# Kernel optimization log

Measured on AMD Instinct MI355X. Metric: run time of the kernel, lower is better.

The kernel has to match this reference:

```python
import jax, jax.numpy as jnp
import numpy as np

E = 16        # n_experts
K = 2         # n_active_experts
D = 2048      # d_model
F = 1408      # ffn_hidden
B, S = 4, 2048


def _swiglu(x, wg, wu, wd):
    # x: [N, D]; wg/wu: [F, D]; wd: [D, F]
    return (jax.nn.silu(x @ wg.T) * (x @ wu.T)) @ wd.T


def setup_inputs() -> dict:
    key = jax.random.key(0)
    ks = jax.random.split(key, 8)
    sc = 0.02
    return {
        "x": jax.random.normal(ks[0], (B, S, D), jnp.float32),
        "gate_w": jax.random.normal(ks[1], (E, D), jnp.float32) * sc,
        "w_gate": jax.random.normal(ks[2], (E, F, D), jnp.float32) * sc,
        "w_up": jax.random.normal(ks[3], (E, F, D), jnp.float32) * sc,
        "w_down": jax.random.normal(ks[4], (E, D, F), jnp.float32) * sc,
        "sw_gate": jax.random.normal(ks[5], (F, D), jnp.float32) * sc,
        "sw_up": jax.random.normal(ks[6], (F, D), jnp.float32) * sc,
        "sw_down": jax.random.normal(ks[7], (D, F), jnp.float32) * sc,
        "expert_bias": jnp.zeros((E,), jnp.float32),
    }


def reference(x, gate_w, w_gate, w_up, w_down, sw_gate, sw_up, sw_down, expert_bias):
    b, s, d = x.shape
    flat = x.reshape(-1, d)                           # [N, D]
    logits = flat @ gate_w.T                          # [N, E]
    probs = jax.nn.softmax(logits, axis=-1)
    biased = logits + expert_bias
    _, top_idx = jax.lax.top_k(biased, K)             # [N, K] int32
    top_w = jnp.take_along_axis(probs, top_idx, axis=-1)
    top_w = top_w / jnp.sum(top_w, axis=-1, keepdims=True)
    # scatter top-k weights into a dense per-expert combine matrix [N, E]
    combine = jnp.sum(jax.nn.one_hot(top_idx, E, dtype=flat.dtype) * top_w[..., None], axis=1)
    out = jnp.zeros_like(flat)
    for e in range(E):  # fixed small expert loop
        out = out + combine[:, e:e + 1] * _swiglu(flat, w_gate[e], w_up[e], w_down[e])
    out = out + _swiglu(flat, sw_gate, sw_up, sw_down)  # shared expert
    return out.reshape(b, s, d)
```

## Files before the change

kernel.cpp:

```cpp
#include <hip/hip_runtime.h>
#include <hip/hip_bf16.h>
#include <cstdint>

#define NE 16
#define D_ 2048
#define F_ 1408
#define NTOK 8192
#define NPAIR (NTOK * 2)
#define SHARED_BASE NPAIR
#define NTOT (NPAIR + NTOK)

#define BM1 256
#define BN1 128
#define BK 64
#define NF1 (F_ / BN1)
#define NF2 (D_ / BN1)
#define MAXRT 111

typedef __attribute__((ext_vector_type(8))) short short8;
typedef __attribute__((ext_vector_type(4))) float f32x4;

static __device__ __forceinline__ ushort f2bf(float f) {
    union { float f; unsigned u; } v; v.f = f;
    unsigned u = v.u;
    return (ushort)((u + 0x7FFFu + ((u >> 16) & 1u)) >> 16);
}

static __device__ __forceinline__ float bf2f(ushort u) {
    union { unsigned u; float f; } v; v.u = ((unsigned)u) << 16;
    return v.f;
}

static __device__ __forceinline__ void cvt_store8(ushort* dst, const float* src) {
    const float4* s = reinterpret_cast<const float4*>(src);
    float4 a = s[0], b = s[1];
    short8 v;
    v[0] = (short)f2bf(a.x); v[1] = (short)f2bf(a.y);
    v[2] = (short)f2bf(a.z); v[3] = (short)f2bf(a.w);
    v[4] = (short)f2bf(b.x); v[5] = (short)f2bf(b.y);
    v[6] = (short)f2bf(b.z); v[7] = (short)f2bf(b.w);
    *reinterpret_cast<short8*>(dst) = v;
}

static __device__ __forceinline__ void gll16(const void* g, void* l) {
    __builtin_amdgcn_global_load_lds((const __attribute__((address_space(1))) void*)g,
                                     (__attribute__((address_space(3))) void*)l, 16, 0, 0);
}

__global__ __launch_bounds__(256) void k_cvt(const float* __restrict__ src,
                                             ushort* __restrict__ dst, int n8) {
    int i = blockIdx.x * 256 + threadIdx.x;
    int stride = gridDim.x * 256;
    for (; i < n8; i += stride) cvt_store8(dst + (size_t)i * 8, src + (size_t)i * 8);
}

__global__ __launch_bounds__(256) void k_route(const float* __restrict__ x,
                                               const float* __restrict__ gate_w,
                                               const float* __restrict__ expert_bias,
                                               int* __restrict__ topk_idx,
                                               float* __restrict__ topk_w) {
    const int wave = threadIdx.x >> 6;
    const int lane = threadIdx.x & 63;
    const int tok = blockIdx.x * 4 + wave;
    if (tok >= NTOK) return;
    const float* xr = x + (size_t)tok * D_;
    float xv[D_ / 64];
#pragma unroll
    for (int i = 0; i < D_ / 64; ++i) xv[i] = xr[lane + 64 * i];

    float logits[NE];
#pragma unroll
    for (int e = 0; e < NE; ++e) {
        const float* gw = gate_w + e * D_;
        float p = 0.f;
#pragma unroll
        for (int i = 0; i < D_ / 64; ++i) p += xv[i] * gw[lane + 64 * i];
#pragma unroll
        for (int off = 32; off > 0; off >>= 1) p += __shfl_xor(p, off, 64);
        logits[e] = p;
    }
    int i1 = 0; float b1 = logits[0] + expert_bias[0];
#pragma unroll
    for (int e = 1; e < NE; ++e) {
        float b = logits[e] + expert_bias[e];
        if (b > b1) { b1 = b; i1 = e; }
    }
    int i2 = -1; float b2 = -3.4e38f;
#pragma unroll
    for (int e = 0; e < NE; ++e) {
        if (e == i1) continue;
        float b = logits[e] + expert_bias[e];
        if (b > b2) { b2 = b; i2 = e; }
    }
    float l1 = logits[i1], l2 = logits[i2];
    float m = fmaxf(l1, l2);
    float e1 = __expf(l1 - m), e2 = __expf(l2 - m);
    float s = e1 + e2;
    if (lane == 0) {
        topk_idx[tok * 2 + 0] = i1;
        topk_idx[tok * 2 + 1] = i2;
        topk_w[tok * 2 + 0] = e1 / s;
        topk_w[tok * 2 + 1] = e2 / s;
    }
}

__global__ void k_zero_meta(int* meta) {
    if (threadIdx.x < 128) meta[threadIdx.x] = 0;
}

__global__ __launch_bounds__(256) void k_count(const int* __restrict__ topk_idx,
                                               int* __restrict__ meta) {
    int t = blockIdx.x * 256 + threadIdx.x;
    if (t >= NTOK) return;
    atomicAdd(&meta[topk_idx[t * 2 + 0]], 1);
    atomicAdd(&meta[topk_idx[t * 2 + 1]], 1);
}

__global__ void k_prefix(int* meta) {
    if (threadIdx.x == 0) {
        int acc = 0;
        for (int e = 0; e < NE; ++e) { meta[32 + e] = acc; acc += meta[e]; }
        meta[32 + NE] = acc;
        int t = 0;
        for (int e = 0; e < NE; ++e) { meta[64 + e] = t; t += (meta[e] + BM1 - 1) / BM1; }
        meta[64 + NE] = t;
        meta[64 + NE + 1] = t + NTOK / BM1;
    }
}

__global__ __launch_bounds__(256) void k_scatter(const int* __restrict__ topk_idx,
                                                 const float* __restrict__ topk_w,
                                                 int* __restrict__ meta,
                                                 int* __restrict__ tok_sorted,
                                                 float* __restrict__ w_sorted,
                                                 int* __restrict__ inv) {
    int t = blockIdx.x * 256 + threadIdx.x;
    if (t >= NTOK) return;
#pragma unroll
    for (int k = 0; k < 2; ++k) {
        int e = topk_idx[t * 2 + k];
        int p = atomicAdd(&meta[16 + e], 1);
        int idx = meta[32 + e] + p;
        tok_sorted[idx] = t;
        w_sorted[idx] = topk_w[t * 2 + k];
        inv[t * 2 + k] = idx;
    }
}

static __device__ __forceinline__ bool grid_decode(const int* meta, int bid, int NF,
                                                   int& e, int& row0, int& fx) {
    if (bid >= meta[64 + NE + 1] * NF) return false;
    e = (bid >= meta[64 + NE] * NF) ? NE : 0;
    if (e == 0) {
#pragma unroll
        for (int i = 1; i < NE; ++i) if (bid >= meta[64 + i] * NF) e = i;
    }
    const int tile_base = meta[64 + e];
    const int nrt = meta[64 + e + 1] - tile_base;
    const int bw = bid - tile_base * NF;
    fx = bw / nrt;
    row0 = (bw - fx * nrt) * BM1;
    return true;
}

__global__ __launch_bounds__(512, 2) void k_ffn1(const ushort* __restrict__ xb,
                                                 const ushort* __restrict__ wgb,
                                                 const ushort* __restrict__ wub,
                                                 const ushort* __restrict__ swgb,
                                                 const ushort* __restrict__ swub,
                                                 const int* __restrict__ meta,
                                                 const int* __restrict__ tok_sorted,
                                                 const float* __restrict__ w_sorted,
                                                 ushort* __restrict__ Hbuf) {
    int e, row0, fx;
    if (!grid_decode(meta, blockIdx.x, NF1, e, row0, fx)) return;
    int n_e, base;
    if (e < NE) { n_e = meta[e]; base = meta[32 + e]; }
    else        { n_e = NTOK;    base = SHARED_BASE; }
    const int f0 = fx * BN1;
    const ushort* wg = (e < NE) ? wgb + (size_t)e * F_ * D_ : swgb;
    const ushort* wu = (e < NE) ? wub + (size_t)e * F_ * D_ : swub;

    __shared__ __align__(16) ushort As[2][BM1 * BK];
    __shared__ __align__(16) ushort Gs[2][BN1 * BK];
    __shared__ __align__(16) ushort Us[2][BN1 * BK];
    __shared__ int tks[BM1];
    __shared__ float tws[BM1];

    const int tid = threadIdx.x;
    const int wv = tid >> 6, lane = tid & 63;
    if (tid < BM1) {
        int r = row0 + tid;
        if (r < n_e) {
            tks[tid] = (e < NE) ? tok_sorted[base + r] : r;
            tws[tid] = (e < NE) ? w_sorted[base + r] : 1.0f;
        } else { tks[tid] = 0; tws[tid] = 0.f; }
    }
    __syncthreads();

    const ushort* srcA[4]; const ushort* srcG[2]; const ushort* srcU[2];
#pragma unroll
    for (int j = 0; j < 4; ++j) {
        int c = j * 512 + wv * 64 + lane;
        int r = c >> 3;
        int col = ((c & 7) ^ (r & 7)) * 8;
        srcA[j] = xb + (size_t)tks[r] * D_ + col;
    }
#pragma unroll
    for (int j = 0; j < 2; ++j) {
        int c = j * 512 + wv * 64 + lane;
        int r = c >> 3;
        int col = ((c & 7) ^ (r & 7)) * 8;
        srcG[j] = wg + (size_t)(f0 + r) * D_ + col;
        srcU[j] = wu + (size_t)(f0 + r) * D_ + col;
    }

    auto stage = [&](int buf, int k0) {
        char* bA = (char*)(&As[buf][0]) + wv * 1024;
        char* bG = (char*)(&Gs[buf][0]) + wv * 1024;
        char* bU = (char*)(&Us[buf][0]) + wv * 1024;
        gll16(srcA[0] + k0, bA);         gll16(srcA[1] + k0, bA + 8192);
        gll16(srcA[2] + k0, bA + 16384); gll16(srcA[3] + k0, bA + 24576);
        gll16(srcG[0] + k0, bG);         gll16(srcG[1] + k0, bG + 8192);
        gll16(srcU[0] + k0, bU);         gll16(srcU[1] + k0, bU + 8192);
    };

    f32x4 accg[4][4] = {}; f32x4 accu[4][4] = {};
    const int wm = (wv >> 1) * 64, wn = (wv & 1) * 64;
    const int fr = lane & 15, fq = lane >> 4;
    const int sw = fr & 7;
    const int rc0 = ((fq ^ sw) * 8);
    const int rc1 = (((4 + fq) ^ sw) * 8);

    auto compute = [&](int buf) {
        const ushort* pA = As[buf];
        const ushort* pG = Gs[buf];
        const ushort* pU = Us[buf];
#pragma unroll
        for (int kk = 0; kk < 2; ++kk) {
            const int rc = kk ? rc1 : rc0;
            short8 af[4], gf[4], uf[4];
#pragma unroll
            for (int mi = 0; mi < 4; ++mi)
                af[mi] = *reinterpret_cast<const short8*>(&pA[(wm + mi * 16 + fr) * BK + rc]);
#pragma unroll
            for (int ni = 0; ni < 4; ++ni) {
                gf[ni] = *reinterpret_cast<const short8*>(&pG[(wn + ni * 16 + fr) * BK + rc]);
                uf[ni] = *reinterpret_cast<const short8*>(&pU[(wn + ni * 16 + fr) * BK + rc]);
            }
#pragma unroll
            for (int mi = 0; mi < 4; ++mi)
#pragma unroll
                for (int ni = 0; ni < 4; ++ni) {
                    accg[mi][ni] = __builtin_amdgcn_mfma_f32_16x16x32_bf16(af[mi], gf[ni], accg[mi][ni], 0, 0, 0);
                    accu[mi][ni] = __builtin_amdgcn_mfma_f32_16x16x32_bf16(af[mi], uf[ni], accu[mi][ni], 0, 0, 0);
                }
        }
    };

    const int NK = D_ / BK;
    stage(0, 0);
    stage(1, BK);
    asm volatile("s_waitcnt vmcnt(8)" ::: "memory");
    __builtin_amdgcn_s_barrier();
    __builtin_amdgcn_sched_barrier(0);
    int cur = 0;
    for (int ks = 0; ks < NK; ++ks) {
        compute(cur);
        __builtin_amdgcn_s_barrier();
        if (ks + 2 < NK) {
            stage(cur, (ks + 2) * BK);
            asm volatile("s_waitcnt vmcnt(8)" ::: "memory");
        } else if (ks + 1 < NK) {
            asm volatile("s_waitcnt vmcnt(0)" ::: "memory");
        }
        __builtin_amdgcn_s_barrier();
        __builtin_amdgcn_sched_barrier(0);
        cur ^= 1;
    }

#pragma unroll
    for (int mi = 0; mi < 4; ++mi) {
#pragma unroll
        for (int r = 0; r < 4; ++r) {
            int lr = wm + mi * 16 + fq * 4 + r;
            int grow = row0 + lr;
            if (grow < n_e) {
                float w = tws[lr];
                ushort* hrow = Hbuf + (size_t)(base + grow) * F_ + f0 + wn;
#pragma unroll
                for (int ni = 0; ni < 4; ++ni) {
                    float g = accg[mi][ni][r];
                    float u = accu[mi][ni][r];
                    float h = w * (g / (1.f + __expf(-g))) * u;
                    hrow[ni * 16 + fr] = f2bf(h);
                }
            }
        }
    }
}

__global__ __launch_bounds__(512, 2) void k_ffn2(const ushort* __restrict__ Hbuf,
                                                 const ushort* __restrict__ wdb,
                                                 const ushort* __restrict__ swdb,
                                                 const int* __restrict__ meta,
                                                 ushort* __restrict__ Obuf) {
    int e, row0, dx;
    if (!grid_decode(meta, blockIdx.x, NF2, e, row0, dx)) return;
    int n_e, base;
    if (e < NE) { n_e = meta[e]; base = meta[32 + e]; }
    else        { n_e = NTOK;    base = SHARED_BASE; }
    const int d0 = dx * BN1;
    const ushort* wd = (e < NE) ? wdb + (size_t)e * D_ * F_ : swdb;

    __shared__ __align__(16) ushort As[2][BM1 * BK];
    __shared__ __align__(16) ushort Bs[2][BN1 * BK];

    const int tid = threadIdx.x;
    const int wv = tid >> 6, lane = tid & 63;

    const ushort* srcA[4]; const ushort* srcB[2];
#pragma unroll
    for (int j = 0; j < 4; ++j) {
        int c = j * 512 + wv * 64 + lane;
        int r = c >> 3;
        int col = ((c & 7) ^ (r & 7)) * 8;
        srcA[j] = Hbuf + (size_t)(base + row0 + r) * F_ + col;
    }
#pragma unroll
    for (int j = 0; j < 2; ++j) {
        int c = j * 512 + wv * 64 + lane;
        int r = c >> 3;
        int col = ((c & 7) ^ (r & 7)) * 8;
        srcB[j] = wd + (size_t)(d0 + r) * F_ + col;
    }

    auto stage = [&](int buf, int k0) {
        char* bA = (char*)(&As[buf][0]) + wv * 1024;
        char* bB = (char*)(&Bs[buf][0]) + wv * 1024;
        gll16(srcA[0] + k0, bA);         gll16(srcA[1] + k0, bA + 8192);
        gll16(srcA[2] + k0, bA + 16384); gll16(srcA[3] + k0, bA + 24576);
        gll16(srcB[0] + k0, bB);         gll16(srcB[1] + k0, bB + 8192);
    };

    f32x4 acc[4][4] = {};
    const int wm = (wv >> 1) * 64, wn = (wv & 1) * 64;
    const int fr = lane & 15, fq = lane >> 4;
    const int sw = fr & 7;
    const int rc0 = ((fq ^ sw) * 8);
    const int rc1 = (((4 + fq) ^ sw) * 8);

    auto compute = [&](int buf) {
        const ushort* pA = As[buf];
        const ushort* pB = Bs[buf];
#pragma unroll
        for (int kk = 0; kk < 2; ++kk) {
            const int rc = kk ? rc1 : rc0;
            short8 af[4], bfr[4];
#pragma unroll
            for (int mi = 0; mi < 4; ++mi)
                af[mi] = *reinterpret_cast<const short8*>(&pA[(wm + mi * 16 + fr) * BK + rc]);
#pragma unroll
            for (int ni = 0; ni < 4; ++ni)
                bfr[ni] = *reinterpret_cast<const short8*>(&pB[(wn + ni * 16 + fr) * BK + rc]);
#pragma unroll
            for (int mi = 0; mi < 4; ++mi)
#pragma unroll
                for (int ni = 0; ni < 4; ++ni)
                    acc[mi][ni] = __builtin_amdgcn_mfma_f32_16x16x32_bf16(af[mi], bfr[ni], acc[mi][ni], 0, 0, 0);
        }
    };

    const int NK = F_ / BK;
    stage(0, 0);
    stage(1, BK);
    asm volatile("s_waitcnt vmcnt(6)" ::: "memory");
    __builtin_amdgcn_s_barrier();
    __builtin_amdgcn_sched_barrier(0);
    int cur = 0;
    for (int ks = 0; ks < NK; ++ks) {
        compute(cur);
        __builtin_amdgcn_s_barrier();
        if (ks + 2 < NK) {
            stage(cur, (ks + 2) * BK);
            asm volatile("s_waitcnt vmcnt(6)" ::: "memory");
        } else if (ks + 1 < NK) {
            asm volatile("s_waitcnt vmcnt(0)" ::: "memory");
        }
        __builtin_amdgcn_s_barrier();
        __builtin_amdgcn_sched_barrier(0);
        cur ^= 1;
    }

#pragma unroll
    for (int mi = 0; mi < 4; ++mi) {
#pragma unroll
        for (int r = 0; r < 4; ++r) {
            int lr = wm + mi * 16 + fq * 4 + r;
            int slot = row0 + lr;
            if (slot < n_e) {
                ushort* orow = Obuf + (size_t)(base + slot) * D_ + d0 + wn;
#pragma unroll
                for (int ni = 0; ni < 4; ++ni)
                    orow[ni * 16 + fr] = f2bf(acc[mi][ni][r]);
            }
        }
    }
}

__global__ __launch_bounds__(256) void k_gather(const ushort* __restrict__ Obuf,
                                                const int* __restrict__ inv,
                                                float* __restrict__ out) {
    const int t = blockIdx.x;
    const int c = threadIdx.x * 8;
    const int s1 = inv[t * 2 + 0];
    const int s2 = inv[t * 2 + 1];
    short8 a = *reinterpret_cast<const short8*>(&Obuf[(size_t)s1 * D_ + c]);
    short8 b = *reinterpret_cast<const short8*>(&Obuf[(size_t)s2 * D_ + c]);
    short8 d = *reinterpret_cast<const short8*>(&Obuf[(size_t)(SHARED_BASE + t) * D_ + c]);
    float4 o0, o1;
    o0.x = bf2f((ushort)a[0]) + bf2f((ushort)b[0]) + bf2f((ushort)d[0]);
    o0.y = bf2f((ushort)a[1]) + bf2f((ushort)b[1]) + bf2f((ushort)d[1]);
    o0.z = bf2f((ushort)a[2]) + bf2f((ushort)b[2]) + bf2f((ushort)d[2]);
    o0.w = bf2f((ushort)a[3]) + bf2f((ushort)b[3]) + bf2f((ushort)d[3]);
    o1.x = bf2f((ushort)a[4]) + bf2f((ushort)b[4]) + bf2f((ushort)d[4]);
    o1.y = bf2f((ushort)a[5]) + bf2f((ushort)b[5]) + bf2f((ushort)d[5]);
    o1.z = bf2f((ushort)a[6]) + bf2f((ushort)b[6]) + bf2f((ushort)d[6]);
    o1.w = bf2f((ushort)a[7]) + bf2f((ushort)b[7]) + bf2f((ushort)d[7]);
    float4* op = reinterpret_cast<float4*>(out + (size_t)t * D_ + c);
    op[0] = o0; op[1] = o1;
}

extern "C" void kernel_launch(void* const* d_in, const int* in_sizes, int n_in,
                              void* d_out, int out_size, void* d_ws, size_t ws_size,
                              hipStream_t stream) {
    const float* x        = (const float*)d_in[0];
    const float* gate_w   = (const float*)d_in[1];
    const float* w_gate   = (const float*)d_in[2];
    const float* w_up     = (const float*)d_in[3];
    const float* w_down   = (const float*)d_in[4];
    const float* sw_gate  = (const float*)d_in[5];
    const float* sw_up    = (const float*)d_in[6];
    const float* sw_down  = (const float*)d_in[7];
    const float* expert_bias = (const float*)d_in[8];
    float* out = (float*)d_out;

    const size_t NW = (size_t)NE * F_ * D_;
    const size_t NSW = (size_t)F_ * D_;
    const size_t NX = (size_t)NTOK * D_;

    char* ws = (char*)d_ws;
    size_t off = 0;
    ushort* xb   = (ushort*)(ws + off); off += NX * 2;
    ushort* wgb  = (ushort*)(ws + off); off += NW * 2;
    ushort* wub  = (ushort*)(ws + off); off += NW * 2;
    ushort* wdb  = (ushort*)(ws + off); off += NW * 2;
    ushort* swgb = (ushort*)(ws + off); off += NSW * 2;
    ushort* swub = (ushort*)(ws + off); off += NSW * 2;
    ushort* swdb = (ushort*)(ws + off); off += NSW * 2;
    ushort* Hbuf = (ushort*)(ws + off); off += (size_t)NTOT * F_ * 2;
    int* tok_sorted = (int*)(ws + off); off += NPAIR * sizeof(int);
    float* w_sorted = (float*)(ws + off); off += NPAIR * sizeof(float);
    int* topk_idx = (int*)(ws + off); off += NTOK * 2 * sizeof(int);
    float* topk_w = (float*)(ws + off); off += NTOK * 2 * sizeof(float);
    int* inv = (int*)(ws + off); off += NTOK * 2 * sizeof(int);
    int* meta = (int*)(ws + off); off += 512;

    ushort* Obuf = wgb;

    k_route<<<NTOK / 4, 256, 0, stream>>>(x, gate_w, expert_bias, topk_idx, topk_w);
    k_zero_meta<<<1, 128, 0, stream>>>(meta);
    k_count<<<NTOK / 256, 256, 0, stream>>>(topk_idx, meta);
    k_prefix<<<1, 1, 0, stream>>>(meta);
    k_scatter<<<NTOK / 256, 256, 0, stream>>>(topk_idx, topk_w, meta, tok_sorted, w_sorted, inv);

    auto cvt = [&](const float* s, ushort* d, size_t n) {
        int n8 = (int)(n / 8);
        int blocks = (n8 + 255) / 256;
        if (blocks > 4096) blocks = 4096;
        k_cvt<<<blocks, 256, 0, stream>>>(s, d, n8);
    };
    cvt(x, xb, NX);
    cvt(w_gate, wgb, NW);
    cvt(w_up, wub, NW);
    cvt(w_down, wdb, NW);
    cvt(sw_gate, swgb, NSW);
    cvt(sw_up, swub, NSW);
    cvt(sw_down, swdb, NSW);

    k_ffn1<<<MAXRT * NF1, 512, 0, stream>>>(xb, wgb, wub, swgb, swub,
                                            meta, tok_sorted, w_sorted, Hbuf);

    k_ffn2<<<MAXRT * NF2, 512, 0, stream>>>(Hbuf, wdb, swdb, meta, Obuf);

    k_gather<<<NTOK, 256, 0, stream>>>(Obuf, inv, out);
}
```

Baseline: 945.1 us.

## Halve K-tile to 32 with new LDS swizzle and raise occupancy to 4 blocks

Cuts the K tile of both FFN GEMM kernels from 64 to 32. The LDS footprint per block halves, so launch bounds now ask for 4 blocks of 512 threads per CU instead of 2. The LDS layout and load addressing are rewritten with a new swizzle (lds_idx) that pairs rows, so each 16x16x32 MFMA fragment load stays free of bank conflicts. The trade-off is twice as many K iterations and barriers, and a tighter register budget that may spill the 128 float accumulators of the gate/up kernel.

```diff
diff --git a/kernel.cpp b/kernel.cpp
--- a/kernel.cpp
+++ b/kernel.cpp
@@ -12,7 +12,7 @@
 
 #define BM1 256
 #define BN1 128
-#define BK 64
+#define BK 32
 #define NF1 (F_ / BN1)
 #define NF2 (D_ / BN1)
 #define MAXRT 111
@@ -45,6 +45,10 @@
 static __device__ __forceinline__ void gll16(const void* g, void* l) {
     __builtin_amdgcn_global_load_lds((const __attribute__((address_space(1))) void*)g,
                                      (__attribute__((address_space(3))) void*)l, 16, 0, 0);
+}
+
+static __device__ __forceinline__ int lds_idx(int r, int fq) {
+    return ((r >> 1) * 8 + (r & 1) * 4 + (fq ^ ((r >> 1) & 3))) * 8;
 }
 
 __global__ __launch_bounds__(256) void k_cvt(const float* __restrict__ src,
@@ -163,7 +167,7 @@
     return true;
 }
 
-__global__ __launch_bounds__(512, 2) void k_ffn1(const ushort* __restrict__ xb,
+__global__ __launch_bounds__(512, 4) void k_ffn1(const ushort* __restrict__ xb,
                                                  const ushort* __restrict__ wgb,
                                                  const ushort* __restrict__ wub,
                                                  const ushort* __restrict__ swgb,
@@ -198,70 +202,67 @@
     }
     __syncthreads();
 
-    const ushort* srcA[4]; const ushort* srcG[2]; const ushort* srcU[2];
-#pragma unroll
-    for (int j = 0; j < 4; ++j) {
-        int c = j * 512 + wv * 64 + lane;
-        int r = c >> 3;
-        int col = ((c & 7) ^ (r & 7)) * 8;
-        srcA[j] = xb + (size_t)tks[r] * D_ + col;
-    }
+    const ushort* srcA[2]; const ushort* srcG; const ushort* srcU;
 #pragma unroll
     for (int j = 0; j < 2; ++j) {
         int c = j * 512 + wv * 64 + lane;
-        int r = c >> 3;
-        int col = ((c & 7) ^ (r & 7)) * 8;
-        srcG[j] = wg + (size_t)(f0 + r) * D_ + col;
-        srcU[j] = wu + (size_t)(f0 + r) * D_ + col;
+        int gr = (c >> 3) * 2 + ((c >> 2) & 1);
+        int gj = (c & 3) ^ ((c >> 3) & 3);
+        srcA[j] = xb + (size_t)tks[gr] * D_ + gj * 8;
+    }
+    {
+        int c = wv * 64 + lane;
+        int gr = (c >> 3) * 2 + ((c >> 2) & 1);
+        int gj = (c & 3) ^ ((c >> 3) & 3);
+        srcG = wg + (size_t)(f0 + gr) * D_ + gj * 8;
+        srcU = wu + (size_t)(f0 + gr) * D_ + gj * 8;
     }
 
     auto stage = [&](int buf, int k0) {
         char* bA = (char*)(&As[buf][0]) + wv * 1024;
         char* bG = (char*)(&Gs[buf][0]) + wv * 1024;
         char* bU = (char*)(&Us[buf][0]) + wv * 1024;
-        gll16(srcA[0] + k0, bA);         gll16(srcA[1] + k0, bA + 8192);
-        gll16(srcA[2] + k0, bA + 16384); gll16(srcA[3] + k0, bA + 24576);
-        gll16(srcG[0] + k0, bG);         gll16(srcG[1] + k0, bG + 8192);
-        gll16(srcU[0] + k0, bU);         gll16(srcU[1] + k0, bU + 8192);
+        gll16(srcA[0] + k0, bA); gll16(srcA[1] + k0, bA + 8192);
+        gll16(srcG + k0, bG);
+        gll16(srcU + k0, bU);
     };
 
     f32x4 accg[4][4] = {}; f32x4 accu[4][4] = {};
     const int wm = (wv >> 1) * 64, wn = (wv & 1) * 64;
     const int fr = lane & 15, fq = lane >> 4;
-    const int sw = fr & 7;
-    const int rc0 = ((fq ^ sw) * 8);
-    const int rc1 = (((4 + fq) ^ sw) * 8);
+
+    int offA[4], offN[4];
+#pragma unroll
+    for (int mi = 0; mi < 4; ++mi) offA[mi] = lds_idx(wm + mi * 16 + fr, fq);
+#pragma unroll
+    for (int ni = 0; ni < 4; ++ni) offN[ni] = lds_idx(wn + ni * 16 + fr, fq);
 
     auto compute = [&](int buf) {
         const ushort* pA = As[buf];
         const ushort* pG = Gs[buf];
         const ushort* pU = Us[buf];
-#pragma unroll
-        for (int kk = 0; kk < 2; ++kk) {
-            const int rc = kk ? rc1 : rc0;
-            short8 af[4], gf[4], uf[4];
-#pragma unroll
-            for (int mi = 0; mi < 4; ++mi)
-                af[mi] = *reinterpret_cast<const short8*>(&pA[(wm + mi * 16 + fr) * BK + rc]);
+        short8 af[4], gf[4], uf[4];
+#pragma unroll
+        for (int mi = 0; mi < 4; ++mi)
+            af[mi] = *reinterpret_cast<const short8*>(&pA[offA[mi]]);
+#pragma unroll
+        for (int ni = 0; ni < 4; ++ni) {
+            gf[ni] = *reinterpret_cast<const short8*>(&pG[offN[ni]]);
+            uf[ni] = *reinterpret_cast<const short8*>(&pU[offN[ni]]);
+        }
+#pragma unroll
+        for (int mi = 0; mi < 4; ++mi)
 #pragma unroll
             for (int ni = 0; ni < 4; ++ni) {
-                gf[ni] = *reinterpret_cast<const short8*>(&pG[(wn + ni * 16 + fr) * BK + rc]);
-                uf[ni] = *reinterpret_cast<const short8*>(&pU[(wn + ni * 16 + fr) * BK + rc]);
+                accg[mi][ni] = __builtin_amdgcn_mfma_f32_16x16x32_bf16(af[mi], gf[ni], accg[mi][ni], 0, 0, 0);
+                accu[mi][ni] = __builtin_amdgcn_mfma_f32_16x16x32_bf16(af[mi], uf[ni], accu[mi][ni], 0, 0, 0);
             }
-#pragma unroll
-            for (int mi = 0; mi < 4; ++mi)
-#pragma unroll
-                for (int ni = 0; ni < 4; ++ni) {
-                    accg[mi][ni] = __builtin_amdgcn_mfma_f32_16x16x32_bf16(af[mi], gf[ni], accg[mi][ni], 0, 0, 0);
-                    accu[mi][ni] = __builtin_amdgcn_mfma_f32_16x16x32_bf16(af[mi], uf[ni], accu[mi][ni], 0, 0, 0);
-                }
-        }
     };
 
     const int NK = D_ / BK;
     stage(0, 0);
     stage(1, BK);
-    asm volatile("s_waitcnt vmcnt(8)" ::: "memory");
+    asm volatile("s_waitcnt vmcnt(4)" ::: "memory");
     __builtin_amdgcn_s_barrier();
     __builtin_amdgcn_sched_barrier(0);
     int cur = 0;
@@ -270,7 +271,7 @@
         __builtin_amdgcn_s_barrier();
         if (ks + 2 < NK) {
             stage(cur, (ks + 2) * BK);
-            asm volatile("s_waitcnt vmcnt(8)" ::: "memory");
+            asm volatile("s_waitcnt vmcnt(4)" ::: "memory");
         } else if (ks + 1 < NK) {
             asm volatile("s_waitcnt vmcnt(0)" ::: "memory");
         }
@@ -300,7 +301,7 @@
     }
 }
 
-__global__ __launch_bounds__(512, 2) void k_ffn2(const ushort* __restrict__ Hbuf,
+__global__ __launch_bounds__(512, 4) void k_ffn2(const ushort* __restrict__ Hbuf,
                                                  const ushort* __restrict__ wdb,
                                                  const ushort* __restrict__ swdb,
                                                  const int* __restrict__ meta,
@@ -319,62 +320,59 @@
     const int tid = threadIdx.x;
     const int wv = tid >> 6, lane = tid & 63;
 
-    const ushort* srcA[4]; const ushort* srcB[2];
-#pragma unroll
-    for (int j = 0; j < 4; ++j) {
-        int c = j * 512 + wv * 64 + lane;
-        int r = c >> 3;
-        int col = ((c & 7) ^ (r & 7)) * 8;
-        srcA[j] = Hbuf + (size_t)(base + row0 + r) * F_ + col;
-    }
+    const ushort* srcA[2]; const ushort* srcB;
 #pragma unroll
     for (int j = 0; j < 2; ++j) {
         int c = j * 512 + wv * 64 + lane;
-        int r = c >> 3;
-        int col = ((c & 7) ^ (r & 7)) * 8;
-        srcB[j] = wd + (size_t)(d0 + r) * F_ + col;
+        int gr = (c >> 3) * 2 + ((c >> 2) & 1);
+        int gj = (c & 3) ^ ((c >> 3) & 3);
+        srcA[j] = Hbuf + (size_t)(base + row0 + gr) * F_ + gj * 8;
+    }
+    {
+        int c = wv * 64 + lane;
+        int gr = (c >> 3) * 2 + ((c >> 2) & 1);
+        int gj = (c & 3) ^ ((c >> 3) & 3);
+        srcB = wd + (size_t)(d0 + gr) * F_ + gj * 8;
     }
 
     auto stage = [&](int buf, int k0) {
         char* bA = (char*)(&As[buf][0]) + wv * 1024;
         char* bB = (char*)(&Bs[buf][0]) + wv * 1024;
-        gll16(srcA[0] + k0, bA);         gll16(srcA[1] + k0, bA + 8192);
-        gll16(srcA[2] + k0, bA + 16384); gll16(srcA[3] + k0, bA + 24576);
-        gll16(srcB[0] + k0, bB);         gll16(srcB[1] + k0, bB + 8192);
+        gll16(srcA[0] + k0, bA); gll16(srcA[1] + k0, bA + 8192);
+        gll16(srcB + k0, bB);
     };
 
     f32x4 acc[4][4] = {};
     const int wm = (wv >> 1) * 64, wn = (wv & 1) * 64;
     const int fr = lane & 15, fq = lane >> 4;
-    const int sw = fr & 7;
-    const int rc0 = ((fq ^ sw) * 8);
-    const int rc1 = (((4 + fq) ^ sw) * 8);
+
+    int offA[4], offN[4];
+#pragma unroll
+    for (int mi = 0; mi < 4; ++mi) offA[mi] = lds_idx(wm + mi * 16 + fr, fq);
+#pragma unroll
+    for (int ni = 0; ni < 4; ++ni) offN[ni] = lds_idx(wn + ni * 16 + fr, fq);
 
     auto compute = [&](int buf) {
         const ushort* pA = As[buf];
         const ushort* pB = Bs[buf];
-#pragma unroll
-        for (int kk = 0; kk < 2; ++kk) {
-            const int rc = kk ? rc1 : rc0;
-            short8 af[4], bfr[4];
-#pragma unroll
-            for (int mi = 0; mi < 4; ++mi)
-                af[mi] = *reinterpret_cast<const short8*>(&pA[(wm + mi * 16 + fr) * BK + rc]);
+        short8 af[4], bfr[4];
+#pragma unroll
+        for (int mi = 0; mi < 4; ++mi)
+            af[mi] = *reinterpret_cast<const short8*>(&pA[offA[mi]]);
+#pragma unroll
+        for (int ni = 0; ni < 4; ++ni)
+            bfr[ni] = *reinterpret_cast<const short8*>(&pB[offN[ni]]);
+#pragma unroll
+        for (int mi = 0; mi < 4; ++mi)
 #pragma unroll
             for (int ni = 0; ni < 4; ++ni)
-                bfr[ni] = *reinterpret_cast<const short8*>(&pB[(wn + ni * 16 + fr) * BK + rc]);
-#pragma unroll
-            for (int mi = 0; mi < 4; ++mi)
-#pragma unroll
-                for (int ni = 0; ni < 4; ++ni)
-                    acc[mi][ni] = __builtin_amdgcn_mfma_f32_16x16x32_bf16(af[mi], bfr[ni], acc[mi][ni], 0, 0, 0);
-        }
+                acc[mi][ni] = __builtin_amdgcn_mfma_f32_16x16x32_bf16(af[mi], bfr[ni], acc[mi][ni], 0, 0, 0);
     };
 
     const int NK = F_ / BK;
     stage(0, 0);
     stage(1, BK);
-    asm volatile("s_waitcnt vmcnt(6)" ::: "memory");
+    asm volatile("s_waitcnt vmcnt(3)" ::: "memory");
     __builtin_amdgcn_s_barrier();
     __builtin_amdgcn_sched_barrier(0);
     int cur = 0;
@@ -383,7 +381,7 @@
         __builtin_amdgcn_s_barrier();
         if (ks + 2 < NK) {
             stage(cur, (ks + 2) * BK);
-            asm volatile("s_waitcnt vmcnt(6)" ::: "memory");
+            asm volatile("s_waitcnt vmcnt(3)" ::: "memory");
         } else if (ks + 1 < NK) {
             asm volatile("s_waitcnt vmcnt(0)" ::: "memory");
         }
```

New measurement: 3.566 ms. 277% more time.

## Fuse x bf16 conversion into routing, batch weight casts, remap blocks per XCD

Applied to the files above, without the earlier changes.

Folds the x-to-bf16 conversion into the routing kernel, which already loads each token row, so the separate x conversion pass is removed. The seven conversion launches become two launches that each convert three tensors. The FFN kernels also remap block indices so consecutive logical tiles land on the same XCD, aiming for better L2 reuse of shared weight and activation tiles. This trades some index arithmetic per element in the conversion kernel and adds a dependence on the hardware's round-robin dispatch of workgroups across XCDs.

```diff
diff --git a/kernel.cpp b/kernel.cpp
--- a/kernel.cpp
+++ b/kernel.cpp
@@ -47,18 +47,36 @@
                                      (__attribute__((address_space(3))) void*)l, 16, 0, 0);
 }
 
-__global__ __launch_bounds__(256) void k_cvt(const float* __restrict__ src,
-                                             ushort* __restrict__ dst, int n8) {
+static __device__ __forceinline__ int xcd_map(int p, int nwg) {
+    int q = nwg >> 3, r = nwg & 7;
+    int x = p & 7, k = p >> 3;
+    int base = (x < r) ? x * (q + 1) : r * (q + 1) + (x - r) * q;
+    return base + k;
+}
+
+template <int N8>
+__global__ __launch_bounds__(256) void k_cvt3(const float* __restrict__ s0,
+                                              const float* __restrict__ s1,
+                                              const float* __restrict__ s2,
+                                              ushort* __restrict__ d0,
+                                              ushort* __restrict__ d1,
+                                              ushort* __restrict__ d2) {
     int i = blockIdx.x * 256 + threadIdx.x;
     int stride = gridDim.x * 256;
-    for (; i < n8; i += stride) cvt_store8(dst + (size_t)i * 8, src + (size_t)i * 8);
+    for (; i < 3 * N8; i += stride) {
+        int t = i / N8, j = i - t * N8;
+        const float* s = (t == 0) ? s0 : (t == 1) ? s1 : s2;
+        ushort* d = (t == 0) ? d0 : (t == 1) ? d1 : d2;
+        cvt_store8(d + (size_t)j * 8, s + (size_t)j * 8);
+    }
 }
 
 __global__ __launch_bounds__(256) void k_route(const float* __restrict__ x,
                                                const float* __restrict__ gate_w,
                                                const float* __restrict__ expert_bias,
                                                int* __restrict__ topk_idx,
-                                               float* __restrict__ topk_w) {
+                                               float* __restrict__ topk_w,
+                                               ushort* __restrict__ xb) {
     const int wave = threadIdx.x >> 6;
     const int lane = threadIdx.x & 63;
     const int tok = blockIdx.x * 4 + wave;
@@ -67,6 +85,10 @@
     float xv[D_ / 64];
 #pragma unroll
     for (int i = 0; i < D_ / 64; ++i) xv[i] = xr[lane + 64 * i];
+
+    ushort* xbr = xb + (size_t)tok * D_;
+#pragma unroll
+    for (int i = 0; i < D_ / 64; ++i) xbr[lane + 64 * i] = f2bf(xv[i]);
 
     float logits[NE];
 #pragma unroll
@@ -173,7 +195,8 @@
                                                  const float* __restrict__ w_sorted,
                                                  ushort* __restrict__ Hbuf) {
     int e, row0, fx;
-    if (!grid_decode(meta, blockIdx.x, NF1, e, row0, fx)) return;
+    const int lbid = xcd_map(blockIdx.x, gridDim.x);
+    if (!grid_decode(meta, lbid, NF1, e, row0, fx)) return;
     int n_e, base;
     if (e < NE) { n_e = meta[e]; base = meta[32 + e]; }
     else        { n_e = NTOK;    base = SHARED_BASE; }
@@ -306,7 +329,8 @@
                                                  const int* __restrict__ meta,
                                                  ushort* __restrict__ Obuf) {
     int e, row0, dx;
-    if (!grid_decode(meta, blockIdx.x, NF2, e, row0, dx)) return;
+    const int lbid = xcd_map(blockIdx.x, gridDim.x);
+    if (!grid_decode(meta, lbid, NF2, e, row0, dx)) return;
     int n_e, base;
     if (e < NE) { n_e = meta[e]; base = meta[32 + e]; }
     else        { n_e = NTOK;    base = SHARED_BASE; }
@@ -468,25 +492,16 @@
 
     ushort* Obuf = wgb;
 
-    k_route<<<NTOK / 4, 256, 0, stream>>>(x, gate_w, expert_bias, topk_idx, topk_w);
+    k_route<<<NTOK / 4, 256, 0, stream>>>(x, gate_w, expert_bias, topk_idx, topk_w, xb);
     k_zero_meta<<<1, 128, 0, stream>>>(meta);
     k_count<<<NTOK / 256, 256, 0, stream>>>(topk_idx, meta);
     k_prefix<<<1, 1, 0, stream>>>(meta);
     k_scatter<<<NTOK / 256, 256, 0, stream>>>(topk_idx, topk_w, meta, tok_sorted, w_sorted, inv);
 
-    auto cvt = [&](const float* s, ushort* d, size_t n) {
-        int n8 = (int)(n / 8);
-        int blocks = (n8 + 255) / 256;
-        if (blocks > 4096) blocks = 4096;
-        k_cvt<<<blocks, 256, 0, stream>>>(s, d, n8);
-    };
-    cvt(x, xb, NX);
-    cvt(w_gate, wgb, NW);
-    cvt(w_up, wub, NW);
-    cvt(w_down, wdb, NW);
-    cvt(sw_gate, swgb, NSW);
-    cvt(sw_up, swub, NSW);
-    cvt(sw_down, swdb, NSW);
+    k_cvt3<(int)(NE * F_ * D_ / 8)><<<4096, 256, 0, stream>>>(w_gate, w_up, w_down,
+                                                              wgb, wub, wdb);
+    k_cvt3<(int)(F_ * D_ / 8)><<<2048, 256, 0, stream>>>(sw_gate, sw_up, sw_down,
+                                                         swgb, swub, swdb);
 
     k_ffn1<<<MAXRT * NF1, 512, 0, stream>>>(xb, wgb, wub, swgb, swub,
                                             meta, tok_sorted, w_sorted, Hbuf);
```

After: 1.011 ms. +7.0%, slower.
